# Optimization experiments

Measured on AMD Instinct MI355X. Metric: run time of the kernel, lower is better.

The kernel has to match this reference:

```python
import jax, jax.numpy as jnp
import numpy as np

DIM, HEADS, NB_FEATURES = 512, 8, 64
HEAD_DIM = DIM // HEADS


def setup_inputs() -> dict:
    key = jax.random.key(0)
    k_x, k_qkv, k_pm, k_wp, k_bp = jax.random.split(key, 5)
    B, N = 8, 4096
    x = jax.random.normal(k_x, (B, N, DIM), dtype=jnp.float32)
    # to_qkv: Linear(dim, 3*dim, bias=False) -> apply as x @ w_qkv
    w_qkv = jax.random.normal(k_qkv, (DIM, 3 * DIM), dtype=jnp.float32) * (1.0 / np.sqrt(DIM))
    # random projection buffer [H, D, F]
    proj_mat = jax.random.normal(k_pm, (HEADS, HEAD_DIM, NB_FEATURES), dtype=jnp.float32)
    # output projection Linear(dim, dim) with bias
    w_proj = jax.random.normal(k_wp, (DIM, DIM), dtype=jnp.float32) * (1.0 / np.sqrt(DIM))
    b_proj = jax.random.normal(k_bp, (DIM,), dtype=jnp.float32) * 0.01
    return {"x": x, "w_qkv": w_qkv, "proj_mat": proj_mat, "w_proj": w_proj, "b_proj": b_proj}


def _phi(t, proj_mat):
    # t: [B,N,H,D], proj_mat: [H,D,F] -> [B,N,H,F]
    return jax.nn.elu(jnp.einsum('bnhd,hdf->bnhf', t, proj_mat)) + 1.0


def reference(x, w_qkv, proj_mat, w_proj, b_proj):
    B, N, dim = x.shape
    H, D = HEADS, dim // HEADS
    qkv = x @ w_qkv  # [B,N,3*dim]
    q, k, v = jnp.split(qkv, 3, axis=-1)
    q = q.reshape(B, N, H, D)
    k = k.reshape(B, N, H, D)
    v = v.reshape(B, N, H, D)
    q_phi = _phi(q, proj_mat)  # [B,N,H,F]
    k_phi = _phi(k, proj_mat)  # [B,N,H,F]
    kv = jnp.einsum('bnhf,bnhd->bhfd', k_phi, v)  # [B,H,F,D]
    z = 1.0 / jnp.einsum('bnhf,bhf->bnh', q_phi, k_phi.sum(axis=1))  # [B,N,H]
    out = jnp.einsum('bnhf,bhfd,bnh->bnhd', q_phi, kv, z)  # [B,N,H,D]
    out = out.reshape(B, N, H * D)
    return out @ w_proj + b_proj
```

## Files before the change

### kernel.cpp

```cpp
#include <hip/hip_runtime.h>
#include <hip/hip_bf16.h>

typedef __bf16 bf16_t;
typedef __bf16 bf16x4 __attribute__((ext_vector_type(4)));
typedef __bf16 bf16x8 __attribute__((ext_vector_type(8)));
typedef float f32x2 __attribute__((ext_vector_type(2)));
typedef float f32x4 __attribute__((ext_vector_type(4)));

__device__ __forceinline__ void gload16(const void* g, void* l) {
  __builtin_amdgcn_global_load_lds((const __attribute__((address_space(1))) void*)g,
                                   (__attribute__((address_space(3))) void*)l, 16, 0, 0);
}

#define VMW(n) asm volatile("s_waitcnt vmcnt(" #n ")" ::: "memory")

__global__ __launch_bounds__(256) void prep_qk(const float* __restrict__ w_qkv,
                                               const float* __restrict__ proj,
                                               bf16_t* __restrict__ WeffT) {
  const int half = blockIdx.x >> 3, h = blockIdx.x & 7;
  const int i0 = blockIdx.y * 64;
  __shared__ float P[64 * 64];
  __shared__ float Wt[64][65];
  const int t = threadIdx.x;
  #pragma unroll
  for (int r = 0; r < 16; ++r) P[t + 256 * r] = proj[(size_t)h * 4096 + t + 256 * r];
  #pragma unroll
  for (int r = 0; r < 16; ++r) {
    const int idx = t + 256 * r;
    Wt[idx >> 6][idx & 63] =
        w_qkv[(size_t)(i0 + (idx >> 6)) * 1536 + half * 512 + h * 64 + (idx & 63)];
  }
  __syncthreads();
  const int i = t & 63, fg = t >> 6;
  for (int f = fg; f < 64; f += 4) {
    float s = 0.f;
    #pragma unroll
    for (int d = 0; d < 64; ++d) s += Wt[i][d] * P[d * 64 + f];
    WeffT[(size_t)(half * 512 + h * 64 + f) * 512 + i0 + i] = (bf16_t)s;
  }
}

__global__ __launch_bounds__(256) void prep_v(const float* __restrict__ w_qkv,
                                              bf16_t* __restrict__ WeffT) {
  __shared__ bf16_t tile[32][33];
  const int i0 = blockIdx.x * 32, n0 = blockIdx.y * 32;
  const int tn = threadIdx.x & 31, ti = threadIdx.x >> 5;
  #pragma unroll
  for (int p = 0; p < 4; ++p) {
    const int i = ti + p * 8;
    tile[i][tn] = (bf16_t)w_qkv[(size_t)(i0 + i) * 1536 + 1024 + n0 + tn];
  }
  __syncthreads();
  #pragma unroll
  for (int p = 0; p < 4; ++p) {
    const int n = ti + p * 8;
    WeffT[(size_t)(1024 + n0 + n) * 512 + i0 + tn] = tile[tn][n];
  }
}

__global__ __launch_bounds__(256) void gemm_qkv(const float* __restrict__ x,
                                                const bf16_t* __restrict__ WeffT,
                                                bf16_t* __restrict__ q_phi,
                                                bf16_t* __restrict__ kT,
                                                bf16_t* __restrict__ vT) {
  __shared__ alignas(16) char smem[49152];
  const int t = threadIdx.x, w = t >> 6, l = t & 63;
  const int hw = blockIdx.x;
  const int bid = (hw & 7) * 384 + (hw >> 3);
  const int tok_blk = bid / 12, cb = bid % 12;
  const size_t tok0 = (size_t)tok_blk * 128;
  const bool qpath = (cb < 4);
  const float* Xp = x + tok0 * 512;
  const bf16_t* Wp = WeffT + (size_t)(qpath ? cb * 128 : 512 + (cb - 4) * 128) * 512;

  const int wr = w >> 1, wc = w & 1;
  const int lrow = l & 15, lkb = l >> 4;

  const int sr8 = t >> 3, su8 = t & 7;
  const int sr4 = t >> 2, su4 = t & 3;
  const size_t fcol = (size_t)((su8 ^ (sr8 & 7)) * 4);
  const size_t hcol = (size_t)((su4 ^ ((t >> 3) & 3)) * 8);

  auto stageF = [&](int s) {
    char* dst = smem + (s & 1) * 16384;
    #pragma unroll
    for (int c = 0; c < 4; ++c)
      gload16(Xp + (size_t)(c * 32 + sr8) * 512 + s * 32 + fcol, dst + c * 4096 + t * 16);
  };
  auto stageH = [&](int s) {
    char* dst = smem + 32768 + (s & 1) * 8192;
    #pragma unroll
    for (int c = 0; c < 2; ++c)
      gload16(Wp + (size_t)(c * 64 + sr4) * 512 + s * 32 + hcol, dst + c * 4096 + t * 16);
  };

  f32x4 acc[4][4];
  #pragma unroll
  for (int m = 0; m < 4; ++m)
    #pragma unroll
    for (int n = 0; n < 4; ++n) acc[m][n] = f32x4{0.f, 0.f, 0.f, 0.f};

  stageF(0); stageH(0);
  __syncthreads();

  for (int kt = 0; kt < 16; ++kt) {
    if (kt + 1 < 16) { stageF(kt + 1); stageH(kt + 1); }
    const char* Fs = smem + (kt & 1) * 16384;
    const char* Hs = smem + 32768 + (kt & 1) * 8192;
    bf16x8 pf[4], qf[4];
    if (qpath) {
      #pragma unroll
      for (int m = 0; m < 4; ++m) {
        const int r = wr * 64 + m * 16 + lrow;
        pf[m] = *(const bf16x8*)(Hs + r * 64 + ((lkb ^ ((r >> 1) & 3)) << 4));
      }
      #pragma unroll
      for (int n = 0; n < 4; ++n) {
        const int r = wc * 64 + n * 16 + lrow;
        const f32x4 a = *(const f32x4*)(Fs + r * 128 + (((2 * lkb) ^ (r & 7)) << 4));
        const f32x4 b = *(const f32x4*)(Fs + r * 128 + (((2 * lkb + 1) ^ (r & 7)) << 4));
        #pragma unroll
        for (int j = 0; j < 4; ++j) { qf[n][j] = (bf16_t)a[j]; qf[n][4 + j] = (bf16_t)b[j]; }
      }
    } else {
      #pragma unroll
      for (int m = 0; m < 4; ++m) {
        const int r = wr * 64 + m * 16 + lrow;
        const f32x4 a = *(const f32x4*)(Fs + r * 128 + (((2 * lkb) ^ (r & 7)) << 4));
        const f32x4 b = *(const f32x4*)(Fs + r * 128 + (((2 * lkb + 1) ^ (r & 7)) << 4));
        #pragma unroll
        for (int j = 0; j < 4; ++j) { pf[m][j] = (bf16_t)a[j]; pf[m][4 + j] = (bf16_t)b[j]; }
      }
      #pragma unroll
      for (int n = 0; n < 4; ++n) {
        const int r = wc * 64 + n * 16 + lrow;
        qf[n] = *(const bf16x8*)(Hs + r * 64 + ((lkb ^ ((r >> 1) & 3)) << 4));
      }
    }
    #pragma unroll
    for (int m = 0; m < 4; ++m)
      #pragma unroll
      for (int n = 0; n < 4; ++n)
        acc[m][n] = __builtin_amdgcn_mfma_f32_16x16x32_bf16(pf[m], qf[n], acc[m][n], 0, 0, 0);
    __syncthreads();
  }

  bf16_t* ep = (bf16_t*)smem;
  const bool doElu = qpath || (cb < 8);
  #pragma unroll
  for (int n = 0; n < 4; ++n) {
    const int qc = wc * 64 + n * 16 + lrow;
    #pragma unroll
    for (int m = 0; m < 4; ++m) {
      const int pr0 = wr * 64 + m * 16 + lkb * 4;
      bf16x4 o;
      #pragma unroll
      for (int j = 0; j < 4; ++j) {
        float v = acc[m][n][j];
        if (doElu) v = v > 0.f ? v + 1.f : __expf(v);
        o[j] = (bf16_t)v;
      }
      const int u = pr0 >> 3;
      *(bf16x4*)((char*)ep + qc * 256 + ((u ^ (qc & 15)) << 4) + (pr0 & 7) * 2) = o;
    }
  }
  __syncthreads();
  #pragma unroll
  for (int i = 0; i < 8; ++i) {
    const int flat = i * 256 + t;
    const int qc2 = flat >> 4, u2 = flat & 15;
    bf16x8 vv = *(const bf16x8*)((char*)ep + qc2 * 256 + ((u2 ^ (qc2 & 15)) << 4));
    if (qpath) {
      *(bf16x8*)&q_phi[(tok0 + qc2) * 512 + cb * 128 + u2 * 8] = vv;
    } else {
      const int f512 = (cb - 4) * 128 + qc2;
      bf16_t* dst = (f512 < 512 ? kT + ((size_t)(tok0 >> 12) * 512 + f512) * 4096
                                : vT + ((size_t)(tok0 >> 12) * 512 + (f512 - 512)) * 4096) +
                    (tok0 & 4095) + u2 * 8;
      *(bf16x8*)dst = vv;
    }
  }
}

__global__ __launch_bounds__(256) void kv_mfma(const bf16_t* __restrict__ kT,
                                               const bf16_t* __restrict__ vT,
                                               float* __restrict__ kv,
                                               float* __restrict__ ksum) {
  const int bh = blockIdx.x;
  const int nbase = blockIdx.y * 512;
  __shared__ alignas(16) char smem[32768];
  const int t = threadIdx.x, w = t >> 6, l = t & 63;
  const int wr = w >> 1, wc = w & 1;
  const int lrow = l & 15, lkb = l >> 4;
  const int st_r = l >> 3;
  const int st_c = ((l & 7) ^ st_r) * 8;
  const bf16_t* Kp = kT + (size_t)bh * 64 * 4096;
  const bf16_t* Vp = vT + (size_t)bh * 64 * 4096;

  f32x4 acc[2][2];
  #pragma unroll
  for (int m = 0; m < 2; ++m)
    #pragma unroll
    for (int n = 0; n < 2; ++n) acc[m][n] = f32x4{0.f, 0.f, 0.f, 0.f};
  float ksf[2] = {0.f, 0.f};

  #pragma unroll
  for (int c = 0; c < 2; ++c) {
    const int q8 = w * 2 + c;
    gload16(Kp + (size_t)(q8 * 8 + st_r) * 4096 + nbase + st_c, smem + q8 * 1024);
    gload16(Vp + (size_t)(q8 * 8 + st_r) * 4096 + nbase + st_c, smem + 8192 + q8 * 1024);
  }
  __syncthreads();

  int cur = 0;
  for (int st = 0; st < 8; ++st) {
    if (st < 7) {
      char* nb = smem + (cur ^ 1) * 16384;
      const int nb2 = nbase + (st + 1) * 64;
      #pragma unroll
      for (int c = 0; c < 2; ++c) {
        const int q8 = w * 2 + c;
        gload16(Kp + (size_t)(q8 * 8 + st_r) * 4096 + nb2 + st_c, nb + q8 * 1024);
        gload16(Vp + (size_t)(q8 * 8 + st_r) * 4096 + nb2 + st_c, nb + 8192 + q8 * 1024);
      }
    }
    const char* KsB = smem + cur * 16384;
    const char* VsB = KsB + 8192;
    bf16x8 af[2][2], bf[2][2];
    #pragma unroll
    for (int m = 0; m < 2; ++m) {
      const int r = wr * 32 + m * 16 + lrow;
      #pragma unroll
      for (int kk = 0; kk < 2; ++kk) {
        const int kb = lkb + kk * 4;
        af[m][kk] = *(const bf16x8*)(KsB + r * 128 + (((kb ^ (r & 7)) & 7) << 4));
      }
    }
    #pragma unroll
    for (int n = 0; n < 2; ++n) {
      const int r = wc * 32 + n * 16 + lrow;
      #pragma unroll
      for (int kk = 0; kk < 2; ++kk) {
        const int kb = lkb + kk * 4;
        bf[n][kk] = *(const bf16x8*)(VsB + r * 128 + (((kb ^ (r & 7)) & 7) << 4));
      }
    }
    #pragma unroll
    for (int m = 0; m < 2; ++m)
      #pragma unroll
      for (int n = 0; n < 2; ++n) {
        acc[m][n] = __builtin_amdgcn_mfma_f32_16x16x32_bf16(af[m][0], bf[n][0], acc[m][n], 0, 0, 0);
        acc[m][n] = __builtin_amdgcn_mfma_f32_16x16x32_bf16(af[m][1], bf[n][1], acc[m][n], 0, 0, 0);
      }
    if (wc == 0) {
      #pragma unroll
      for (int m = 0; m < 2; ++m)
        #pragma unroll
        for (int kk = 0; kk < 2; ++kk)
          #pragma unroll
          for (int j = 0; j < 8; ++j) ksf[m] += (float)af[m][kk][j];
    }
    __syncthreads();
    cur ^= 1;
  }

  float* kvp = kv + (size_t)bh * 4096;
  #pragma unroll
  for (int m = 0; m < 2; ++m)
    #pragma unroll
    for (int n = 0; n < 2; ++n)
      #pragma unroll
      for (int j = 0; j < 4; ++j)
        atomicAdd(&kvp[(wr * 32 + m * 16 + lkb * 4 + j) * 64 + wc * 32 + n * 16 + lrow],
                  acc[m][n][j]);
  if (wc == 0) {
    #pragma unroll
    for (int m = 0; m < 2; ++m) {
      float s = ksf[m];
      s += __shfl_xor(s, 16);
      s += __shfl_xor(s, 32);
      if (l < 16) atomicAdd(&ksum[(size_t)bh * 64 + wr * 32 + m * 16 + l], s);
    }
  }
}

__global__ __launch_bounds__(256) void w2_kernel(const float* __restrict__ kv,
                                                 const float* __restrict__ w_proj,
                                                 bf16_t* __restrict__ W2T) {
  const int bh = blockIdx.x, b = bh >> 3, h = bh & 7;
  const int j0 = blockIdx.y * 64;
  const int t = threadIdx.x;
  __shared__ float kvs[64][64];
  __shared__ float wps[64][64];
  const float* kvp = kv + (size_t)bh * 4096;
  #pragma unroll
  for (int i = 0; i < 16; ++i) ((float*)kvs)[t + 256 * i] = kvp[t + 256 * i];
  {
    const int d = t >> 2, c16 = (t & 3) * 16;
    const float* src = w_proj + (size_t)(h * 64 + d) * 512 + j0 + c16;
    #pragma unroll
    for (int j = 0; j < 16; ++j) wps[d][c16 + j] = src[j];
  }
  __syncthreads();
  const int fq = t >> 4, jq = t & 15;
  float acc[4][4] = {};
  for (int d = 0; d < 64; ++d) {
    float kf[4], wj[4];
    #pragma unroll
    for (int i = 0; i < 4; ++i) kf[i] = kvs[fq * 4 + i][d];
    #pragma unroll
    for (int i = 0; i < 4; ++i) wj[i] = wps[d][jq * 4 + i];
    #pragma unroll
    for (int i = 0; i < 4; ++i)
      #pragma unroll
      for (int j = 0; j < 4; ++j) acc[i][j] += kf[i] * wj[j];
  }
  #pragma unroll
  for (int j = 0; j < 4; ++j)
    #pragma unroll
    for (int i = 0; i < 4; ++i)
      W2T[((size_t)b * 512 + j0 + jq * 4 + j) * 512 + h * 64 + fq * 4 + i] = (bf16_t)acc[i][j];
}

__global__ __launch_bounds__(256) void gemm_out(const bf16_t* __restrict__ W2T,
                                                const bf16_t* __restrict__ q_phi,
                                                const float* __restrict__ ksum,
                                                float* __restrict__ Cout,
                                                const float* __restrict__ bias) {
  __shared__ alignas(16) char smem[67584];
  const int t = threadIdx.x, w = t >> 6, l = t & 63;
  const int hw = blockIdx.x;
  const int bid = (hw & 7) * 128 + (hw >> 3);
  const int z = bid >> 7;
  const int rem = bid & 127;
  const int qblk = rem >> 2, pblk = rem & 3;
  const size_t tok0 = (size_t)qblk * 128;
  const int pj0 = pblk * 128;
  const bf16_t* Pp = W2T + ((size_t)z * 512 + pj0) * 512;

  const int wr = w >> 1, wc = w & 1;
  const int lrow = l & 15, lkb = l >> 4;
  const int st_r = l >> 3;
  const int st_c = ((l & 7) ^ st_r) * 8;
  const int token = t >> 1, half = t & 1;
  float* ks_lds = (float*)(smem + 65536);

  bf16x8 breg[4];
  auto loadB = [&](int c) {
    const bf16_t* p = q_phi + ((size_t)z * 4096 + tok0 + token) * 512 + c * 64 + half * 32;
    breg[0] = *(const bf16x8*)p;
    breg[1] = *(const bf16x8*)(p + 8);
    breg[2] = *(const bf16x8*)(p + 16);
    breg[3] = *(const bf16x8*)(p + 24);
  };
  auto stageA = [&](int s) {
    #pragma unroll
    for (int c = 0; c < 4; ++c) {
      const int q8 = c * 4 + w;
      gload16(Pp + (size_t)(q8 * 8 + st_r) * 512 + s * 64 + st_c,
              smem + (s & 1) * 16384 + q8 * 1024);
    }
  };
  auto procB = [&](int c) {
    const f32x4* ksv = (const f32x4*)(ks_lds + c * 64 + half * 32);
    float vals[32];
    float dot = 0.f;
    #pragma unroll
    for (int g = 0; g < 8; ++g) {
      const f32x4 kk = ksv[g];
      #pragma unroll
      for (int j = 0; j < 4; ++j) {
        const float v = (float)breg[g >> 1][(g & 1) * 4 + j];
        vals[g * 4 + j] = v;
        dot += v * kk[j];
      }
    }
    dot += __shfl_xor(dot, 1);
    const float zz = 1.f / dot;
    char* dst = smem + 32768 + (c & 1) * 16384;
    #pragma unroll
    for (int g = 0; g < 4; ++g) {
      bf16x8 o;
      #pragma unroll
      for (int j = 0; j < 8; ++j) o[j] = (bf16_t)(vals[g * 8 + j] * zz);
      const int uk = half * 4 + g;
      *(bf16x8*)(dst + token * 128 + ((uk ^ (token & 7)) << 4)) = o;
    }
  };

  {
    const f32x2 kk = *(const f32x2*)&ksum[(size_t)z * 512 + t * 2];
    *(f32x2*)&ks_lds[t * 2] = kk;
  }
  __syncthreads();
  loadB(0);
  stageA(0);
  procB(0);
  VMW(0);
  __syncthreads();

  f32x4 acc[4][4];
  #pragma unroll
  for (int m = 0; m < 4; ++m)
    #pragma unroll
    for (int n = 0; n < 4; ++n) acc[m][n] = f32x4{0.f, 0.f, 0.f, 0.f};

  for (int kt = 0; kt < 8; ++kt) {
    const char* PsB = smem + (kt & 1) * 16384;
    const char* QsB = smem + 32768 + (kt & 1) * 16384;
    bf16x8 pf[4][2], qf[4][2];
    #pragma unroll
    for (int m = 0; m < 4; ++m) {
      const int r = wr * 64 + m * 16 + lrow;
      #pragma unroll
      for (int kk = 0; kk < 2; ++kk) {
        const int kb = lkb + kk * 4;
        pf[m][kk] = *(const bf16x8*)(PsB + r * 128 + (((kb ^ (r & 7)) & 7) << 4));
      }
    }
    #pragma unroll
    for (int n = 0; n < 4; ++n) {
      const int r = wc * 64 + n * 16 + lrow;
      #pragma unroll
      for (int kk = 0; kk < 2; ++kk) {
        const int kb = lkb + kk * 4;
        qf[n][kk] = *(const bf16x8*)(QsB + r * 128 + (((kb ^ (r & 7)) & 7) << 4));
      }
    }
    if (kt + 1 < 8) { loadB(kt + 1); stageA(kt + 1); }
    #pragma unroll
    for (int m = 0; m < 4; ++m)
      #pragma unroll
      for (int n = 0; n < 4; ++n) {
        acc[m][n] = __builtin_amdgcn_mfma_f32_16x16x32_bf16(pf[m][0], qf[n][0], acc[m][n], 0, 0, 0);
        acc[m][n] = __builtin_amdgcn_mfma_f32_16x16x32_bf16(pf[m][1], qf[n][1], acc[m][n], 0, 0, 0);
      }
    if (kt + 1 < 8) { procB(kt + 1); VMW(0); }
    __syncthreads();
  }

  float* ep = (float*)smem;
  #pragma unroll
  for (int p = 0; p < 2; ++p) {
    if (p) __syncthreads();
    #pragma unroll
    for (int nn2 = 0; nn2 < 2; ++nn2) {
      const int n = p * 2 + nn2;
      const int r6 = wc * 32 + (n & 1) * 16 + lrow;
      #pragma unroll
      for (int m = 0; m < 4; ++m) {
        const int pr0 = wr * 64 + m * 16 + lkb * 4;
        f32x4 v = acc[m][n];
        const f32x4 bv = *(const f32x4*)&bias[pj0 + pr0];
        #pragma unroll
        for (int j = 0; j < 4; ++j) v[j] += bv[j];
        const int u = pr0 >> 2;
        *(f32x4*)((char*)ep + r6 * 512 + ((u ^ (r6 & 31)) << 4)) = v;
      }
    }
    __syncthreads();
    #pragma unroll
    for (int i = 0; i < 8; ++i) {
      const int flat = i * 256 + t;
      const int r6 = flat >> 5, u2 = flat & 31;
      f32x4 v = *(const f32x4*)((char*)ep + r6 * 512 + ((u2 ^ (r6 & 31)) << 4));
      const int qc = (r6 >> 5) * 64 + p * 32 + (r6 & 31);
      *(f32x4*)&Cout[((size_t)z * 4096 + tok0 + qc) * 512 + pj0 + u2 * 4] = v;
    }
  }
}

extern "C" void kernel_launch(void* const* d_in, const int* in_sizes, int n_in,
                              void* d_out, int out_size, void* d_ws, size_t ws_size,
                              hipStream_t stream) {
  const float* x      = (const float*)d_in[0];
  const float* w_qkv  = (const float*)d_in[1];
  const float* proj   = (const float*)d_in[2];
  const float* w_proj = (const float*)d_in[3];
  const float* b_proj = (const float*)d_in[4];
  float* out = (float*)d_out;
  char* ws = (char*)d_ws;

  bf16_t* WeffT = (bf16_t*)(ws + 0);
  bf16_t* q_phi = (bf16_t*)(ws + 1572864);
  bf16_t* kT    = (bf16_t*)(ws + 35127296);
  bf16_t* vT    = (bf16_t*)(ws + 68681728);
  float*  kv    = (float*)(ws + 102236160);
  float*  ksum  = (float*)(ws + 103284736);
  bf16_t* W2T   = (bf16_t*)(ws + 103301120);

  prep_qk<<<dim3(16, 8), 256, 0, stream>>>(w_qkv, proj, WeffT);
  prep_v<<<dim3(16, 16), 256, 0, stream>>>(w_qkv, WeffT);
  gemm_qkv<<<3072, 256, 0, stream>>>(x, WeffT, q_phi, kT, vT);
  hipMemsetAsync(kv, 0, 1048576 + 16384, stream);
  kv_mfma<<<dim3(64, 8), 256, 0, stream>>>(kT, vT, kv, ksum);
  w2_kernel<<<dim3(64, 8), 256, 0, stream>>>(kv, w_proj, W2T);
  gemm_out<<<1024, 256, 0, stream>>>(W2T, q_phi, ksum, out, b_proj);
}
```

Before: 169.9 us.

## Double gemm_qkv block to 512 threads with 64-wide K stages

Restructures the QKV GEMM to use 8 waves per block (4x2 wave grid with 32x64 wave tiles) and doubles the K chunk per pipeline stage from 32 to 64. Each stage now issues two MFMAs per accumulator, which halves the number of barriers and loop iterations. The LDS swizzles are adjusted to the wider rows. Shared memory rises to 96 KB and launch_bounds(512,1) is set, so occupancy is limited to about one block per CU and latency hiding depends on the larger block.

```diff
diff --git a/kernel.cpp b/kernel.cpp
--- a/kernel.cpp
+++ b/kernel.cpp
@@ -58,13 +58,16 @@
   }
 }
 
-__global__ __launch_bounds__(256) void gemm_qkv(const float* __restrict__ x,
-                                                const bf16_t* __restrict__ WeffT,
-                                                bf16_t* __restrict__ q_phi,
-                                                bf16_t* __restrict__ kT,
-                                                bf16_t* __restrict__ vT) {
-  __shared__ alignas(16) char smem[49152];
-  const int t = threadIdx.x, w = t >> 6, l = t & 63;
+__global__ __launch_bounds__(512, 1) void gemm_qkv(const float* __restrict__ x,
+                                                   const bf16_t* __restrict__ WeffT,
+                                                   bf16_t* __restrict__ q_phi,
+                                                   bf16_t* __restrict__ kT,
+                                                   bf16_t* __restrict__ vT) {
+  __shared__ alignas(16) char smem[98304];
+  const int t = threadIdx.x;
+  const int wid = t >> 6, l = t & 63;
+  const int wr3 = wid >> 1, wc1 = wid & 1;
+  const int lrow = l & 15, lkb = l >> 4;
   const int hw = blockIdx.x;
   const int bid = (hw & 7) * 384 + (hw >> 3);
   const int tok_blk = bid / 12, cb = bid % 12;
@@ -73,75 +76,76 @@
   const float* Xp = x + tok0 * 512;
   const bf16_t* Wp = WeffT + (size_t)(qpath ? cb * 128 : 512 + (cb - 4) * 128) * 512;
 
-  const int wr = w >> 1, wc = w & 1;
-  const int lrow = l & 15, lkb = l >> 4;
-
-  const int sr8 = t >> 3, su8 = t & 7;
-  const int sr4 = t >> 2, su4 = t & 3;
-  const size_t fcol = (size_t)((su8 ^ (sr8 & 7)) * 4);
-  const size_t hcol = (size_t)((su4 ^ ((t >> 3) & 3)) * 8);
-
-  auto stageF = [&](int s) {
-    char* dst = smem + (s & 1) * 16384;
+  const int f_row = t >> 4;
+  const int f_u = (t & 15) ^ ((t >> 4) & 7);
+  const int h_row = t >> 3;
+  const int h_u = (t & 7) ^ ((t >> 3) & 7);
+
+  auto stage = [&](int s) {
+    char* Fd = smem + (s & 1) * 32768;
     #pragma unroll
     for (int c = 0; c < 4; ++c)
-      gload16(Xp + (size_t)(c * 32 + sr8) * 512 + s * 32 + fcol, dst + c * 4096 + t * 16);
+      gload16(Xp + (size_t)(c * 32 + f_row) * 512 + s * 64 + f_u * 4, Fd + c * 8192 + t * 16);
+    char* Hd = smem + 65536 + (s & 1) * 16384;
+    #pragma unroll
+    for (int c = 0; c < 2; ++c)
+      gload16(Wp + (size_t)(c * 64 + h_row) * 512 + s * 64 + h_u * 8, Hd + c * 8192 + t * 16);
   };
-  auto stageH = [&](int s) {
-    char* dst = smem + 32768 + (s & 1) * 8192;
-    #pragma unroll
-    for (int c = 0; c < 2; ++c)
-      gload16(Wp + (size_t)(c * 64 + sr4) * 512 + s * 32 + hcol, dst + c * 4096 + t * 16);
-  };
-
-  f32x4 acc[4][4];
-  #pragma unroll
-  for (int m = 0; m < 4; ++m)
+
+  f32x4 acc[2][4];
+  #pragma unroll
+  for (int m = 0; m < 2; ++m)
     #pragma unroll
     for (int n = 0; n < 4; ++n) acc[m][n] = f32x4{0.f, 0.f, 0.f, 0.f};
 
-  stageF(0); stageH(0);
-  __syncthreads();
-
-  for (int kt = 0; kt < 16; ++kt) {
-    if (kt + 1 < 16) { stageF(kt + 1); stageH(kt + 1); }
-    const char* Fs = smem + (kt & 1) * 16384;
-    const char* Hs = smem + 32768 + (kt & 1) * 8192;
-    bf16x8 pf[4], qf[4];
-    if (qpath) {
-      #pragma unroll
-      for (int m = 0; m < 4; ++m) {
-        const int r = wr * 64 + m * 16 + lrow;
-        pf[m] = *(const bf16x8*)(Hs + r * 64 + ((lkb ^ ((r >> 1) & 3)) << 4));
-      }
+  stage(0);
+  __syncthreads();
+
+  for (int kt = 0; kt < 8; ++kt) {
+    if (kt + 1 < 8) stage(kt + 1);
+    const char* Fs = smem + (kt & 1) * 32768;
+    const char* Hs = smem + 65536 + (kt & 1) * 16384;
+    bf16x8 pf[2][2], qf[4][2];
+    #pragma unroll
+    for (int kk = 0; kk < 2; ++kk) {
+      const int kb = lkb + kk * 4;
+      if (qpath) {
+        #pragma unroll
+        for (int m = 0; m < 2; ++m) {
+          const int r = wr3 * 32 + m * 16 + lrow;
+          pf[m][kk] = *(const bf16x8*)(Hs + r * 128 + ((kb ^ (r & 7)) << 4));
+        }
+        #pragma unroll
+        for (int n = 0; n < 4; ++n) {
+          const int r = wc1 * 64 + n * 16 + lrow;
+          const f32x4 a = *(const f32x4*)(Fs + r * 256 + (((2 * kb) ^ (r & 7)) << 4));
+          const f32x4 b = *(const f32x4*)(Fs + r * 256 + (((2 * kb + 1) ^ (r & 7)) << 4));
+          #pragma unroll
+          for (int j = 0; j < 4; ++j) { qf[n][kk][j] = (bf16_t)a[j]; qf[n][kk][4 + j] = (bf16_t)b[j]; }
+        }
+      } else {
+        #pragma unroll
+        for (int m = 0; m < 2; ++m) {
+          const int r = wr3 * 32 + m * 16 + lrow;
+          const f32x4 a = *(const f32x4*)(Fs + r * 256 + (((2 * kb) ^ (r & 7)) << 4));
+          const f32x4 b = *(const f32x4*)(Fs + r * 256 + (((2 * kb + 1) ^ (r & 7)) << 4));
+          #pragma unroll
+          for (int j = 0; j < 4; ++j) { pf[m][kk][j] = (bf16_t)a[j]; pf[m][kk][4 + j] = (bf16_t)b[j]; }
+        }
+        #pragma unroll
+        for (int n = 0; n < 4; ++n) {
+          const int r = wc1 * 64 + n * 16 + lrow;
+          qf[n][kk] = *(const bf16x8*)(Hs + r * 128 + ((kb ^ (r & 7)) << 4));
+        }
+      }
+    }
+    #pragma unroll
+    for (int m = 0; m < 2; ++m)
       #pragma unroll
       for (int n = 0; n < 4; ++n) {
-        const int r = wc * 64 + n * 16 + lrow;
-        const f32x4 a = *(const f32x4*)(Fs + r * 128 + (((2 * lkb) ^ (r & 7)) << 4));
-        const f32x4 b = *(const f32x4*)(Fs + r * 128 + (((2 * lkb + 1) ^ (r & 7)) << 4));
-        #pragma unroll
-        for (int j = 0; j < 4; ++j) { qf[n][j] = (bf16_t)a[j]; qf[n][4 + j] = (bf16_t)b[j]; }
-      }
-    } else {
-      #pragma unroll
-      for (int m = 0; m < 4; ++m) {
-        const int r = wr * 64 + m * 16 + lrow;
-        const f32x4 a = *(const f32x4*)(Fs + r * 128 + (((2 * lkb) ^ (r & 7)) << 4));
-        const f32x4 b = *(const f32x4*)(Fs + r * 128 + (((2 * lkb + 1) ^ (r & 7)) << 4));
-        #pragma unroll
-        for (int j = 0; j < 4; ++j) { pf[m][j] = (bf16_t)a[j]; pf[m][4 + j] = (bf16_t)b[j]; }
-      }
-      #pragma unroll
-      for (int n = 0; n < 4; ++n) {
-        const int r = wc * 64 + n * 16 + lrow;
-        qf[n] = *(const bf16x8*)(Hs + r * 64 + ((lkb ^ ((r >> 1) & 3)) << 4));
-      }
-    }
-    #pragma unroll
-    for (int m = 0; m < 4; ++m)
-      #pragma unroll
-      for (int n = 0; n < 4; ++n)
-        acc[m][n] = __builtin_amdgcn_mfma_f32_16x16x32_bf16(pf[m], qf[n], acc[m][n], 0, 0, 0);
+        acc[m][n] = __builtin_amdgcn_mfma_f32_16x16x32_bf16(pf[m][0], qf[n][0], acc[m][n], 0, 0, 0);
+        acc[m][n] = __builtin_amdgcn_mfma_f32_16x16x32_bf16(pf[m][1], qf[n][1], acc[m][n], 0, 0, 0);
+      }
     __syncthreads();
   }
 
@@ -149,10 +153,10 @@
   const bool doElu = qpath || (cb < 8);
   #pragma unroll
   for (int n = 0; n < 4; ++n) {
-    const int qc = wc * 64 + n * 16 + lrow;
-    #pragma unroll
-    for (int m = 0; m < 4; ++m) {
-      const int pr0 = wr * 64 + m * 16 + lkb * 4;
+    const int qc = wc1 * 64 + n * 16 + lrow;
+    #pragma unroll
+    for (int m = 0; m < 2; ++m) {
+      const int pr0 = wr3 * 32 + m * 16 + lkb * 4;
       bf16x4 o;
       #pragma unroll
       for (int j = 0; j < 4; ++j) {
@@ -166,8 +170,8 @@
   }
   __syncthreads();
   #pragma unroll
-  for (int i = 0; i < 8; ++i) {
-    const int flat = i * 256 + t;
+  for (int i = 0; i < 4; ++i) {
+    const int flat = i * 512 + t;
     const int qc2 = flat >> 4, u2 = flat & 15;
     bf16x8 vv = *(const bf16x8*)((char*)ep + qc2 * 256 + ((u2 ^ (qc2 & 15)) << 4));
     if (qpath) {
@@ -491,7 +495,7 @@
 
   prep_qk<<<dim3(16, 8), 256, 0, stream>>>(w_qkv, proj, WeffT);
   prep_v<<<dim3(16, 16), 256, 0, stream>>>(w_qkv, WeffT);
-  gemm_qkv<<<3072, 256, 0, stream>>>(x, WeffT, q_phi, kT, vT);
+  gemm_qkv<<<3072, 512, 0, stream>>>(x, WeffT, q_phi, kT, vT);
   hipMemsetAsync(kv, 0, 1048576 + 16384, stream);
   kv_mfma<<<dim3(64, 8), 256, 0, stream>>>(kT, vT, kv, ksum);
   w2_kernel<<<dim3(64, 8), 256, 0, stream>>>(kv, w_proj, W2T);
```

New measurement: 193.8 us. 14.1% more time.

## Fuse KV reduction into QKV GEMM epilogue, drop kT/vT intermediates

Applied to the files above, without the earlier changes.

Non-Q blocks of the QKV GEMM now compute one head's k_phi (64 cols) and v (64 cols) together, then do the per-tile k_phi^T·v product and k_phi column sums from shared memory with MFMA. Partial results are atomically added into kv/ksum. This removes the separate kv_mfma kernel and the round trip of kT/vT through global memory. In exchange there are many more fp32 atomics (one set per 128-token tile rather than per 512) and extra epilogue work in the GEMM.

```diff
diff --git a/kernel.cpp b/kernel.cpp
--- a/kernel.cpp
+++ b/kernel.cpp
@@ -61,8 +61,8 @@
 __global__ __launch_bounds__(256) void gemm_qkv(const float* __restrict__ x,
                                                 const bf16_t* __restrict__ WeffT,
                                                 bf16_t* __restrict__ q_phi,
-                                                bf16_t* __restrict__ kT,
-                                                bf16_t* __restrict__ vT) {
+                                                float* __restrict__ kv,
+                                                float* __restrict__ ksum) {
   __shared__ alignas(16) char smem[49152];
   const int t = threadIdx.x, w = t >> 6, l = t & 63;
   const int hw = blockIdx.x;
@@ -70,8 +70,17 @@
   const int tok_blk = bid / 12, cb = bid % 12;
   const size_t tok0 = (size_t)tok_blk * 128;
   const bool qpath = (cb < 4);
+  const int head = cb - 4;
   const float* Xp = x + tok0 * 512;
-  const bf16_t* Wp = WeffT + (size_t)(qpath ? cb * 128 : 512 + (cb - 4) * 128) * 512;
+  const bf16_t* Wp0;
+  const bf16_t* Wp1;
+  if (qpath) {
+    Wp0 = WeffT + (size_t)cb * 128 * 512;
+    Wp1 = Wp0 + (size_t)64 * 512;
+  } else {
+    Wp0 = WeffT + (size_t)(512 + head * 64) * 512;
+    Wp1 = WeffT + (size_t)(1024 + head * 64) * 512;
+  }
 
   const int wr = w >> 1, wc = w & 1;
   const int lrow = l & 15, lkb = l >> 4;
@@ -89,9 +98,8 @@
   };
   auto stageH = [&](int s) {
     char* dst = smem + 32768 + (s & 1) * 8192;
-    #pragma unroll
-    for (int c = 0; c < 2; ++c)
-      gload16(Wp + (size_t)(c * 64 + sr4) * 512 + s * 32 + hcol, dst + c * 4096 + t * 16);
+    gload16(Wp0 + (size_t)sr4 * 512 + s * 32 + hcol, dst + t * 16);
+    gload16(Wp1 + (size_t)sr4 * 512 + s * 32 + hcol, dst + 4096 + t * 16);
   };
 
   f32x4 acc[4][4];
@@ -146,10 +154,10 @@
   }
 
   bf16_t* ep = (bf16_t*)smem;
-  const bool doElu = qpath || (cb < 8);
   #pragma unroll
   for (int n = 0; n < 4; ++n) {
     const int qc = wc * 64 + n * 16 + lrow;
+    const bool de = qpath || (qc < 64);
     #pragma unroll
     for (int m = 0; m < 4; ++m) {
       const int pr0 = wr * 64 + m * 16 + lkb * 4;
@@ -157,7 +165,7 @@
       #pragma unroll
       for (int j = 0; j < 4; ++j) {
         float v = acc[m][n][j];
-        if (doElu) v = v > 0.f ? v + 1.f : __expf(v);
+        if (de) v = v > 0.f ? v + 1.f : __expf(v);
         o[j] = (bf16_t)v;
       }
       const int u = pr0 >> 3;
@@ -165,121 +173,54 @@
     }
   }
   __syncthreads();
-  #pragma unroll
-  for (int i = 0; i < 8; ++i) {
-    const int flat = i * 256 + t;
-    const int qc2 = flat >> 4, u2 = flat & 15;
-    bf16x8 vv = *(const bf16x8*)((char*)ep + qc2 * 256 + ((u2 ^ (qc2 & 15)) << 4));
-    if (qpath) {
+  if (qpath) {
+    #pragma unroll
+    for (int i = 0; i < 8; ++i) {
+      const int flat = i * 256 + t;
+      const int qc2 = flat >> 4, u2 = flat & 15;
+      bf16x8 vv = *(const bf16x8*)((char*)ep + qc2 * 256 + ((u2 ^ (qc2 & 15)) << 4));
       *(bf16x8*)&q_phi[(tok0 + qc2) * 512 + cb * 128 + u2 * 8] = vv;
-    } else {
-      const int f512 = (cb - 4) * 128 + qc2;
-      bf16_t* dst = (f512 < 512 ? kT + ((size_t)(tok0 >> 12) * 512 + f512) * 4096
-                                : vT + ((size_t)(tok0 >> 12) * 512 + (f512 - 512)) * 4096) +
-                    (tok0 & 4095) + u2 * 8;
-      *(bf16x8*)dst = vv;
-    }
-  }
-}
-
-__global__ __launch_bounds__(256) void kv_mfma(const bf16_t* __restrict__ kT,
-                                               const bf16_t* __restrict__ vT,
-                                               float* __restrict__ kv,
-                                               float* __restrict__ ksum) {
-  const int bh = blockIdx.x;
-  const int nbase = blockIdx.y * 512;
-  __shared__ alignas(16) char smem[32768];
-  const int t = threadIdx.x, w = t >> 6, l = t & 63;
-  const int wr = w >> 1, wc = w & 1;
-  const int lrow = l & 15, lkb = l >> 4;
-  const int st_r = l >> 3;
-  const int st_c = ((l & 7) ^ st_r) * 8;
-  const bf16_t* Kp = kT + (size_t)bh * 64 * 4096;
-  const bf16_t* Vp = vT + (size_t)bh * 64 * 4096;
-
-  f32x4 acc[2][2];
-  #pragma unroll
-  for (int m = 0; m < 2; ++m)
-    #pragma unroll
-    for (int n = 0; n < 2; ++n) acc[m][n] = f32x4{0.f, 0.f, 0.f, 0.f};
-  float ksf[2] = {0.f, 0.f};
-
-  #pragma unroll
-  for (int c = 0; c < 2; ++c) {
-    const int q8 = w * 2 + c;
-    gload16(Kp + (size_t)(q8 * 8 + st_r) * 4096 + nbase + st_c, smem + q8 * 1024);
-    gload16(Vp + (size_t)(q8 * 8 + st_r) * 4096 + nbase + st_c, smem + 8192 + q8 * 1024);
-  }
-  __syncthreads();
-
-  int cur = 0;
-  for (int st = 0; st < 8; ++st) {
-    if (st < 7) {
-      char* nb = smem + (cur ^ 1) * 16384;
-      const int nb2 = nbase + (st + 1) * 64;
-      #pragma unroll
-      for (int c = 0; c < 2; ++c) {
-        const int q8 = w * 2 + c;
-        gload16(Kp + (size_t)(q8 * 8 + st_r) * 4096 + nb2 + st_c, nb + q8 * 1024);
-        gload16(Vp + (size_t)(q8 * 8 + st_r) * 4096 + nb2 + st_c, nb + 8192 + q8 * 1024);
-      }
-    }
-    const char* KsB = smem + cur * 16384;
-    const char* VsB = KsB + 8192;
-    bf16x8 af[2][2], bf[2][2];
-    #pragma unroll
-    for (int m = 0; m < 2; ++m) {
-      const int r = wr * 32 + m * 16 + lrow;
-      #pragma unroll
-      for (int kk = 0; kk < 2; ++kk) {
-        const int kb = lkb + kk * 4;
-        af[m][kk] = *(const bf16x8*)(KsB + r * 128 + (((kb ^ (r & 7)) & 7) << 4));
-      }
-    }
-    #pragma unroll
-    for (int n = 0; n < 2; ++n) {
-      const int r = wc * 32 + n * 16 + lrow;
-      #pragma unroll
-      for (int kk = 0; kk < 2; ++kk) {
-        const int kb = lkb + kk * 4;
-        bf[n][kk] = *(const bf16x8*)(VsB + r * 128 + (((kb ^ (r & 7)) & 7) << 4));
-      }
-    }
-    #pragma unroll
-    for (int m = 0; m < 2; ++m)
-      #pragma unroll
-      for (int n = 0; n < 2; ++n) {
-        acc[m][n] = __builtin_amdgcn_mfma_f32_16x16x32_bf16(af[m][0], bf[n][0], acc[m][n], 0, 0, 0);
-        acc[m][n] = __builtin_amdgcn_mfma_f32_16x16x32_bf16(af[m][1], bf[n][1], acc[m][n], 0, 0, 0);
-      }
-    if (wc == 0) {
-      #pragma unroll
-      for (int m = 0; m < 2; ++m)
+    }
+  } else {
+    f32x4 acc2[4];
+    #pragma unroll
+    for (int m2 = 0; m2 < 4; ++m2) acc2[m2] = f32x4{0.f, 0.f, 0.f, 0.f};
+    float ks2[4] = {0.f, 0.f, 0.f, 0.f};
+    #pragma unroll
+    for (int ks = 0; ks < 4; ++ks) {
+      const int u = ks * 4 + lkb;
+      bf16x8 af2[4], bf2;
+      #pragma unroll
+      for (int m2 = 0; m2 < 4; ++m2) {
+        const int fr = m2 * 16 + lrow;
+        af2[m2] = *(const bf16x8*)((char*)ep + fr * 256 + ((u ^ (fr & 15)) << 4));
+      }
+      {
+        const int fr = 64 + w * 16 + lrow;
+        bf2 = *(const bf16x8*)((char*)ep + fr * 256 + ((u ^ (fr & 15)) << 4));
+      }
+      #pragma unroll
+      for (int m2 = 0; m2 < 4; ++m2) {
+        acc2[m2] = __builtin_amdgcn_mfma_f32_16x16x32_bf16(af2[m2], bf2, acc2[m2], 0, 0, 0);
         #pragma unroll
-        for (int kk = 0; kk < 2; ++kk)
-          #pragma unroll
-          for (int j = 0; j < 8; ++j) ksf[m] += (float)af[m][kk][j];
-    }
-    __syncthreads();
-    cur ^= 1;
-  }
-
-  float* kvp = kv + (size_t)bh * 4096;
-  #pragma unroll
-  for (int m = 0; m < 2; ++m)
-    #pragma unroll
-    for (int n = 0; n < 2; ++n)
+        for (int j = 0; j < 8; ++j) ks2[m2] += (float)af2[m2][j];
+      }
+    }
+    const int bh = (int)(tok0 >> 12) * 8 + head;
+    float* kvp = kv + (size_t)bh * 4096;
+    #pragma unroll
+    for (int m2 = 0; m2 < 4; ++m2)
       #pragma unroll
       for (int j = 0; j < 4; ++j)
-        atomicAdd(&kvp[(wr * 32 + m * 16 + lkb * 4 + j) * 64 + wc * 32 + n * 16 + lrow],
-                  acc[m][n][j]);
-  if (wc == 0) {
-    #pragma unroll
-    for (int m = 0; m < 2; ++m) {
-      float s = ksf[m];
-      s += __shfl_xor(s, 16);
-      s += __shfl_xor(s, 32);
-      if (l < 16) atomicAdd(&ksum[(size_t)bh * 64 + wr * 32 + m * 16 + l], s);
+        atomicAdd(&kvp[(m2 * 16 + lkb * 4 + j) * 64 + w * 16 + lrow], acc2[m2][j]);
+    if (w == 0) {
+      #pragma unroll
+      for (int m2 = 0; m2 < 4; ++m2) {
+        float s = ks2[m2];
+        s += __shfl_xor(s, 16);
+        s += __shfl_xor(s, 32);
+        if (l < 16) atomicAdd(&ksum[(size_t)bh * 64 + m2 * 16 + l], s);
+      }
     }
   }
 }
@@ -483,17 +424,14 @@
 
   bf16_t* WeffT = (bf16_t*)(ws + 0);
   bf16_t* q_phi = (bf16_t*)(ws + 1572864);
-  bf16_t* kT    = (bf16_t*)(ws + 35127296);
-  bf16_t* vT    = (bf16_t*)(ws + 68681728);
-  float*  kv    = (float*)(ws + 102236160);
-  float*  ksum  = (float*)(ws + 103284736);
-  bf16_t* W2T   = (bf16_t*)(ws + 103301120);
+  float*  kv    = (float*)(ws + 35127296);
+  float*  ksum  = (float*)(ws + 36175872);
+  bf16_t* W2T   = (bf16_t*)(ws + 36192256);
 
   prep_qk<<<dim3(16, 8), 256, 0, stream>>>(w_qkv, proj, WeffT);
   prep_v<<<dim3(16, 16), 256, 0, stream>>>(w_qkv, WeffT);
-  gemm_qkv<<<3072, 256, 0, stream>>>(x, WeffT, q_phi, kT, vT);
   hipMemsetAsync(kv, 0, 1048576 + 16384, stream);
-  kv_mfma<<<dim3(64, 8), 256, 0, stream>>>(kT, vT, kv, ksum);
+  gemm_qkv<<<3072, 256, 0, stream>>>(x, WeffT, q_phi, kv, ksum);
   w2_kernel<<<dim3(64, 8), 256, 0, stream>>>(kv, w_proj, W2T);
   gemm_out<<<1024, 256, 0, stream>>>(W2T, q_phi, ksum, out, b_proj);
 }
```

Result: faster. 166.4 us (-2.1%).
